# Optimization experiments

Measured on AMD Instinct MI355X. Metric: run time of the kernel, lower is better.

## Reference

```python
import math
import jax, jax.numpy as jnp
import numpy as np

B, C, K, P, STRIDE, ITERS = 32, 32, 3, 4, 2, 3
PSIZE = P * P
EPS = 1e-6
LAMBDA = 1e-3
LN_2PI = math.log(2.0 * math.pi)


def _extract_patches(x, K, stride):
    # Replicates torch F.unfold + transpose + view exactly, including the
    # layout reinterpretation: unfold's channel dim is ordered (c, kh, kw)
    # (c slowest) but the torch code views it as (K*K, c).
    b, h, w, c = x.shape
    pad = K // 2
    oh = (h + 2 * pad - K) // stride + 1
    ow = (w + 2 * pad - K) // stride + 1
    xp = jnp.pad(x, ((0, 0), (pad, pad), (pad, pad), (0, 0)))
    sl = []
    for kh in range(K):
        for kw in range(K):
            sl.append(xp[:, kh:kh + stride * (oh - 1) + 1:stride,
                            kw:kw + stride * (ow - 1) + 1:stride, :])
    p = jnp.stack(sl, axis=-1)                 # (b, oh, ow, c, K*K)  -> (c, kh, kw) order
    p = p.reshape(b, oh, ow, c * K * K)        # flat, c slowest (matches torch unfold memory)
    patches = p.reshape(b, oh, ow, K * K, c)   # reinterpret as (K*K, c), as the torch view does
    return patches, oh, ow


def _em_routing(v, a_in, beta_u, beta_a):
    # v: (b, Bin, C, psize), a_in: (b, Bin, 1)
    b, Bin, Cc, psize = v.shape
    r = jnp.full((b, Bin, Cc, 1), 1.0 / Cc, dtype=v.dtype)
    a4 = a_in[:, :, None, :]                   # (b, Bin, 1, 1)
    a_out = None
    mu = None
    for t in range(ITERS):
        # ---- M step ----
        rr = r * a4
        rr = rr / (jnp.sum(rr, axis=2, keepdims=True) + EPS)
        r_sum = jnp.sum(rr, axis=1, keepdims=True)            # (b,1,C,1)
        coeff = rr / (r_sum + EPS)
        mu = jnp.sum(coeff * v, axis=1, keepdims=True)        # (b,1,C,psize)
        sigma_sq = jnp.sum(coeff * (v - mu) ** 2, axis=1, keepdims=True) + EPS
        sigma_sq = jnp.maximum(sigma_sq, 1e-4)
        r_sum_flat = r_sum.reshape(b, Cc, 1)
        sig_flat = jnp.maximum(sigma_sq.reshape(b, Cc, psize), 1e-4)
        cost_h = (beta_u.reshape(1, Cc, 1) + jnp.log(jnp.sqrt(sig_flat))) * r_sum_flat
        a_out = jax.nn.sigmoid(LAMBDA * (beta_a.reshape(1, Cc) - jnp.sum(cost_h, axis=2)))
        a_out = jnp.clip(a_out, 1e-4, 1.0 - 1e-4)
        mu = jnp.nan_to_num(mu, nan=0.0, posinf=1e4, neginf=-1e4)
        sigma_sq = jnp.nan_to_num(sigma_sq, nan=1e-4, posinf=1e4, neginf=1e-4)
        a_out = jnp.nan_to_num(a_out, nan=0.5, posinf=1.0 - 1e-4, neginf=1e-4)
        # ---- E step ----
        if t < ITERS - 1:
            ss = jnp.maximum(sigma_sq, 1e-4)
            ao = jnp.clip(a_out, 1e-4, 1.0 - 1e-4)
            ln_p = -(v - mu) ** 2 / (2.0 * ss) - jnp.log(jnp.sqrt(ss)) - 0.5 * LN_2PI
            ln_ap = jnp.sum(ln_p, axis=3) + jnp.log(ao.reshape(b, 1, Cc) + EPS)
            ln_ap = jnp.nan_to_num(ln_ap, nan=0.0, posinf=50.0, neginf=-50.0)
            r = jax.nn.softmax(ln_ap, axis=2)[..., None]
            r = jnp.nan_to_num(r, nan=1.0 / Cc, posinf=1.0, neginf=0.0)
    p_out = jnp.nan_to_num(mu[:, 0], nan=0.0, posinf=1e4, neginf=-1e4)  # (b, C, psize)
    a_out = jnp.nan_to_num(a_out, nan=0.5, posinf=1.0 - 1e-4, neginf=1e-4)
    return p_out, a_out


def setup_inputs() -> dict:
    key = jax.random.key(0)
    k1, k2 = jax.random.split(key)
    x = jax.random.normal(k1, (2, 16, 16, B * (PSIZE + 1)), dtype=jnp.float32)
    weights = jax.random.normal(k2, (1, K * K * B, C, PSIZE, PSIZE), dtype=jnp.float32) * 0.02
    beta_u = jnp.zeros((C,), dtype=jnp.float32)
    beta_a = jnp.zeros((C,), dtype=jnp.float32)
    return {"x": x, "weights": weights, "beta_u": beta_u, "beta_a": beta_a}


def reference(x, weights, beta_u, beta_a):
    b, h, w, c = x.shape
    patches, oh, ow = _extract_patches(x, K, STRIDE)          # (b,oh,ow,K*K,c)
    p_in = patches[..., :B * PSIZE].reshape(b * oh * ow, K * K * B, PSIZE)
    a_in = patches[..., B * PSIZE:].reshape(b * oh * ow, K * K * B, 1)
    w0 = weights[0]                                           # (K*K*B, C, psize, psize)
    v = jnp.einsum('bip,icpq->bicq', p_in, w0)                # (b*, K*K*B, C, psize)
    p_out, a_out = _em_routing(v, a_in, beta_u, beta_a)
    p_out = p_out.reshape(b, oh, ow, C * PSIZE)
    a_out = a_out.reshape(b, oh, ow, C)
    out = jnp.concatenate([p_out, a_out], axis=3)
    return p_out, a_out, out
```

## Files before the change

kernel.cpp:

```cpp
#include <hip/hip_runtime.h>
#include <hip/hip_bf16.h>
#include <math.h>

#define EPSV 1e-6f
#define LAMBDAV 1e-3f
#define LN_2PI 1.8378770664093453f

__device__ __forceinline__ float bflo(unsigned int u) {
    union { unsigned int i; float f; } x; x.i = u << 16; return x.f;
}
__device__ __forceinline__ float bfhi(unsigned int u) {
    union { unsigned int i; float f; } x; x.i = u & 0xffff0000u; return x.f;
}
__device__ __forceinline__ unsigned short f2bf(float f) {
    __hip_bfloat16 h = __float2bfloat16(f);
    return *(unsigned short*)&h;
}

typedef __attribute__((ext_vector_type(8))) short s8v;
typedef __attribute__((ext_vector_type(4))) float f4v;

__global__ __launch_bounds__(256)
void conv_v_kernel(const float* __restrict__ x, const float* __restrict__ w,
                   __hip_bfloat16* __restrict__ vout)
{
    __shared__ unsigned short wb[512 * 40];
    __shared__ unsigned short pb[128 * 40];

    const int i2  = blockIdx.x;
    const int tid = threadIdx.x;

    for (int u = tid; u < 512 * 8; u += 256) {
        int r = u >> 3, j = u & 7;
        *(unsigned int*)&wb[r * 40 + 16 + j * 2] = 0;
    }
    for (int u = tid; u < 128 * 8; u += 256) {
        int r = u >> 3, j = u & 7;
        *(unsigned int*)&pb[r * 40 + 16 + j * 2] = 0;
    }
    #pragma unroll 4
    for (int u = 0; u < 32; ++u) {
        int idx = u * 256 + tid;
        int c = idx >> 8, p = (idx >> 4) & 15, q = idx & 15;
        wb[(c * 16 + q) * 40 + p] = f2bf(w[(size_t)i2 * 8192 + idx]);
    }
    #pragma unroll
    for (int u = 0; u < 8; ++u) {
        int idx = u * 256 + tid;
        int nn = idx >> 4, p = idx & 15;
        int e  = i2 * 16 + p;
        int k2 = e >> 9, c2 = e & 511;
        int f  = k2 * 544 + c2;
        int ci = f / 9, kk = f - ci * 9;
        int bi = nn >> 6, oi = (nn >> 3) & 7, oj = nn & 7;
        int row = 2 * oi + kk / 3 - 1;
        int col = 2 * oj + (kk - (kk / 3) * 3) - 1;
        float val = 0.f;
        if ((unsigned)row < 16u && (unsigned)col < 16u)
            val = x[((bi * 16 + row) * 16 + col) * 544 + ci];
        pb[nn * 40 + p] = f2bf(val);
    }
    __syncthreads();

    const int lane = tid & 63;
    const int wv   = tid >> 6;
    const int l16  = lane & 15;
    const int quad = lane >> 4;
    const int cq0  = wv * 128;

    s8v afrag[8], bfrag[8];
    #pragma unroll
    for (int mt = 0; mt < 8; ++mt)
        afrag[mt] = *(const s8v*)&wb[(cq0 + mt * 16 + l16) * 40 + quad * 8];
    #pragma unroll
    for (int nt = 0; nt < 8; ++nt)
        bfrag[nt] = *(const s8v*)&pb[(nt * 16 + l16) * 40 + quad * 8];

    #pragma unroll
    for (int nt = 0; nt < 8; ++nt) {
        const int nl = nt * 16 + l16;
        #pragma unroll
        for (int mt = 0; mt < 8; ++mt) {
            f4v acc = {0.f, 0.f, 0.f, 0.f};
            acc = __builtin_amdgcn_mfma_f32_16x16x32_bf16(afrag[mt], bfrag[nt], acc, 0, 0, 0);
            int cq = cq0 + mt * 16 + quad * 4;
            unsigned int lo = f2bf(acc[0]) | ((unsigned int)f2bf(acc[1]) << 16);
            unsigned int hi = f2bf(acc[2]) | ((unsigned int)f2bf(acc[3]) << 16);
            uint2 pk; pk.x = lo; pk.y = hi;
            *(uint2*)((unsigned short*)vout + ((size_t)nl * 288 + i2) * 512 + cq) = pk;
        }
    }
}

__global__ __launch_bounds__(1024, 4)
void em_routing_kernel(const float* __restrict__ x,
                       const unsigned short* __restrict__ v,
                       const float* __restrict__ beta_u,
                       const float* __restrict__ beta_a,
                       float* __restrict__ out)
{
    __shared__ float fct_s[288];
    __shared__ float red_s[16 * 64 * 17];
    __shared__ float mu_s[32 * 17];
    __shared__ float i2ss_s[32 * 17];
    __shared__ float hlog_s[32 * 17];
    __shared__ float rsum_s[32];
    __shared__ float aout_s[32];
    __shared__ float kc_s[32];

    const int n   = blockIdx.x;
    const int tid = threadIdx.x;
    const int bi = n >> 6, oi = (n >> 3) & 7, oj = n & 7;

    if (tid < 288) {
        int k2 = tid >> 5;
        int c2 = 512 + (tid & 31);
        int f  = k2 * 544 + c2;
        int ci = f / 9;
        int kk = f - ci * 9;
        int row = 2 * oi + kk / 3 - 1;
        int col = 2 * oj + (kk - (kk / 3) * 3) - 1;
        float a = 0.f;
        if ((unsigned)row < 16u && (unsigned)col < 16u)
            a = x[((bi * 16 + row) * 16 + col) * 544 + ci];
        fct_s[tid] = a / (a + EPSV);
    }
    __syncthreads();

    const unsigned short* vb = v + (size_t)n * 288 * 512;
    const int wv   = tid >> 6;
    const int lane = tid & 63;
    const int c    = lane & 31;
    const int qh   = lane >> 5;
    const int qb   = qh * 8;
    const unsigned short* base = vb + c * 16 + qb;

    for (int t = 0; t < 3; ++t) {
        float mu8[8], is8[8], kcv = 0.f;
        if (t > 0) {
            #pragma unroll
            for (int j = 0; j < 8; ++j) {
                mu8[j] = mu_s[c * 17 + qb + j];
                is8[j] = i2ss_s[c * 17 + qb + j];
            }
            kcv = kc_s[c];
        }

        float s0 = 0.f, s1[8], s2[8];
        #pragma unroll
        for (int j = 0; j < 8; ++j) { s1[j] = 0.f; s2[j] = 0.f; }

        uint4 ua = *(const uint4*)(base + (size_t)(0 * 16 + wv) * 512);
        uint4 ub = *(const uint4*)(base + (size_t)(1 * 16 + wv) * 512);

        for (int kp = 0; kp < 9; ++kp) {
            const int ia = (2 * kp) * 16 + wv;
            const int ib = (2 * kp + 1) * 16 + wv;
            uint4 una, unb;
            if (kp < 8) {
                una = *(const uint4*)(base + (size_t)((2 * kp + 2) * 16 + wv) * 512);
                unb = *(const uint4*)(base + (size_t)((2 * kp + 3) * 16 + wv) * 512);
            }
            float va[8], vvb[8];
            va[0] = bflo(ua.x); va[1] = bfhi(ua.x);
            va[2] = bflo(ua.y); va[3] = bfhi(ua.y);
            va[4] = bflo(ua.z); va[5] = bfhi(ua.z);
            va[6] = bflo(ua.w); va[7] = bfhi(ua.w);
            vvb[0] = bflo(ub.x); vvb[1] = bfhi(ub.x);
            vvb[2] = bflo(ub.y); vvb[3] = bfhi(ub.y);
            vvb[4] = bflo(ub.z); vvb[5] = bfhi(ub.z);
            vvb[6] = bflo(ub.w); vvb[7] = bfhi(ub.w);

            float rra, rrb;
            if (t == 0) {
                rra = fct_s[ia] * 0.03125f;
                rrb = fct_s[ib] * 0.03125f;
            } else {
                float pa = 0.f, pb2 = 0.f;
                #pragma unroll
                for (int j = 0; j < 8; ++j) {
                    float da = va[j] - mu8[j];
                    float db = vvb[j] - mu8[j];
                    pa  += da * da * is8[j];
                    pb2 += db * db * is8[j];
                }
                pa  += __shfl_xor(pa, 32, 64);
                pb2 += __shfl_xor(pb2, 32, 64);
                float acca = kcv - pa;
                float accb = kcv - pb2;
                float mxa = acca, mxb = accb;
                mxa = fmaxf(mxa, __shfl_xor(mxa, 1, 32));  mxb = fmaxf(mxb, __shfl_xor(mxb, 1, 32));
                mxa = fmaxf(mxa, __shfl_xor(mxa, 2, 32));  mxb = fmaxf(mxb, __shfl_xor(mxb, 2, 32));
                mxa = fmaxf(mxa, __shfl_xor(mxa, 4, 32));  mxb = fmaxf(mxb, __shfl_xor(mxb, 4, 32));
                mxa = fmaxf(mxa, __shfl_xor(mxa, 8, 32));  mxb = fmaxf(mxb, __shfl_xor(mxb, 8, 32));
                mxa = fmaxf(mxa, __shfl_xor(mxa, 16, 32)); mxb = fmaxf(mxb, __shfl_xor(mxb, 16, 32));
                float ea = __expf(acca - mxa);
                float eb = __expf(accb - mxb);
                float sa = ea, sb = eb;
                sa += __shfl_xor(sa, 1, 32);  sb += __shfl_xor(sb, 1, 32);
                sa += __shfl_xor(sa, 2, 32);  sb += __shfl_xor(sb, 2, 32);
                sa += __shfl_xor(sa, 4, 32);  sb += __shfl_xor(sb, 4, 32);
                sa += __shfl_xor(sa, 8, 32);  sb += __shfl_xor(sb, 8, 32);
                sa += __shfl_xor(sa, 16, 32); sb += __shfl_xor(sb, 16, 32);
                rra = (ea / sa) * fct_s[ia];
                rrb = (eb / sb) * fct_s[ib];
            }

            s0 += rra + rrb;
            #pragma unroll
            for (int j = 0; j < 8; ++j) {
                s1[j] += rra * va[j] + rrb * vvb[j];
                s2[j] += rra * va[j] * va[j] + rrb * vvb[j] * vvb[j];
            }
            ua = una; ub = unb;
        }

        {
            float* dst = &red_s[(wv * 64 + lane) * 17];
            dst[0] = s0;
            #pragma unroll
            for (int j = 0; j < 8; ++j) { dst[1 + j] = s1[j]; dst[9 + j] = s2[j]; }
        }
        __syncthreads();

        if (tid < 512) {
            int c2 = tid >> 4, q2 = tid & 15;
            int qh2 = q2 >> 3, j2 = q2 & 7;
            float S0 = 0.f, S1 = 0.f, S2 = 0.f;
            #pragma unroll
            for (int wvi = 0; wvi < 16; ++wvi) {
                S0 += red_s[(wvi * 64 + c2) * 17];
                const float* sp = &red_s[(wvi * 64 + qh2 * 32 + c2) * 17];
                S1 += sp[1 + j2];
                S2 += sp[9 + j2];
            }
            if (q2 == 0) rsum_s[c2] = S0;
            float invr = 1.0f / (S0 + EPSV);
            float w0  = S0 * invr;
            float m   = S1 * invr;
            float s2p = S2 * invr;
            float sig = s2p - m * m * (2.0f - w0);
            sig = fmaxf(sig + EPSV, 1e-4f);
            float hl = 0.5f * logf(sig);
            mu_s[c2 * 17 + q2]   = m;
            hlog_s[c2 * 17 + q2] = hl;
            i2ss_s[c2 * 17 + q2] = 1.0f / (2.0f * sig);
        }
        __syncthreads();

        if (tid < 32) {
            float cs = 0.f, shl = 0.f;
            float bu = beta_u[tid];
            #pragma unroll
            for (int q = 0; q < 16; ++q) { float hl = hlog_s[tid * 17 + q]; shl += hl; cs += bu + hl; }
            cs *= rsum_s[tid];
            float arg = LAMBDAV * (beta_a[tid] - cs);
            float ao  = 1.0f / (1.0f + expf(-arg));
            ao = fminf(fmaxf(ao, 1e-4f), 1.0f - 1e-4f);
            aout_s[tid] = ao;
            kc_s[tid]   = logf(ao + EPSV) - shl - 8.0f * LN_2PI;
        }
        __syncthreads();
    }

    if (tid < 512) {
        int c2 = tid >> 4, q2 = tid & 15;
        float mu = mu_s[c2 * 17 + q2];
        if (isnan(mu)) mu = 0.f;
        mu = fminf(fmaxf(mu, -10000.f), 10000.f);
        out[(size_t)n * 512 + tid] = mu;
        out[69632 + (size_t)n * 544 + tid] = mu;
        if (tid < 32) {
            float ao = aout_s[tid];
            if (isnan(ao)) ao = 0.5f;
            out[65536 + n * 32 + tid] = ao;
            out[69632 + n * 544 + 512 + tid] = ao;
        }
    }
}

extern "C" void kernel_launch(void* const* d_in, const int* in_sizes, int n_in,
                              void* d_out, int out_size, void* d_ws, size_t ws_size,
                              hipStream_t stream) {
    const float* x  = (const float*)d_in[0];
    const float* w  = (const float*)d_in[1];
    const float* bu = (const float*)d_in[2];
    const float* ba = (const float*)d_in[3];
    float* out = (float*)d_out;
    __hip_bfloat16* v = (__hip_bfloat16*)d_ws;

    conv_v_kernel<<<dim3(288), dim3(256), 0, stream>>>(x, w, v);
    em_routing_kernel<<<dim3(128), dim3(1024), 0, stream>>>(
        x, (const unsigned short*)v, bu, ba, out);
}
```

Measured before the change: 130.8 us.

## Remap EM routing lanes to full capsule vectors and use DPP reductions

Each lane now handles all 16 pose elements of one output capsule for a single input row, with the two wave halves processing alternate rows. Before, lanes split the pose elements in half and each covered two rows. This removes the cross-half shuffle inside the softmax, replaces shuffle-based 32-lane max/sum reductions with DPP moves plus a ds_swizzle, and folds the per-capsule activation computation into the 512-thread reduction through a 16-lane DPP sum, which drops one __syncthreads per iteration. The cost is higher register pressure from 16-element accumulators and an extra cross-half shuffle reduction of 33 values before writing to shared memory.

Measured after the change: 131.2 us. About the same (+0.3%).

```diff
diff --git a/kernel.cpp b/kernel.cpp
--- a/kernel.cpp
+++ b/kernel.cpp
@@ -19,6 +19,35 @@
 
 typedef __attribute__((ext_vector_type(8))) short s8v;
 typedef __attribute__((ext_vector_type(4))) float f4v;
+
+template<int CTRL>
+__device__ __forceinline__ float dpp_mv(float x) {
+    return __int_as_float(__builtin_amdgcn_update_dpp(
+        0, __float_as_int(x), CTRL, 0xF, 0xF, true));
+}
+__device__ __forceinline__ float red_max32(float x) {
+    x = fmaxf(x, dpp_mv<0xB1>(x));
+    x = fmaxf(x, dpp_mv<0x4E>(x));
+    x = fmaxf(x, dpp_mv<0x124>(x));
+    x = fmaxf(x, dpp_mv<0x128>(x));
+    x = fmaxf(x, __int_as_float(__builtin_amdgcn_ds_swizzle(__float_as_int(x), 0x401F)));
+    return x;
+}
+__device__ __forceinline__ float red_sum32(float x) {
+    x += dpp_mv<0xB1>(x);
+    x += dpp_mv<0x4E>(x);
+    x += dpp_mv<0x124>(x);
+    x += dpp_mv<0x128>(x);
+    x += __int_as_float(__builtin_amdgcn_ds_swizzle(__float_as_int(x), 0x401F));
+    return x;
+}
+__device__ __forceinline__ float red_sum16(float x) {
+    x += dpp_mv<0xB1>(x);
+    x += dpp_mv<0x4E>(x);
+    x += dpp_mv<0x124>(x);
+    x += dpp_mv<0x128>(x);
+    return x;
+}
 
 __global__ __launch_bounds__(256)
 void conv_v_kernel(const float* __restrict__ x, const float* __restrict__ w,
@@ -100,11 +129,9 @@
                        float* __restrict__ out)
 {
     __shared__ float fct_s[288];
-    __shared__ float red_s[16 * 64 * 17];
+    __shared__ float red_s[16 * 32 * 34];
     __shared__ float mu_s[32 * 17];
     __shared__ float i2ss_s[32 * 17];
-    __shared__ float hlog_s[32 * 17];
-    __shared__ float rsum_s[32];
     __shared__ float aout_s[32];
     __shared__ float kc_s[32];
 
@@ -131,110 +158,96 @@
     const int wv   = tid >> 6;
     const int lane = tid & 63;
     const int c    = lane & 31;
-    const int qh   = lane >> 5;
-    const int qb   = qh * 8;
-    const unsigned short* base = vb + c * 16 + qb;
+    const int half = lane >> 5;
+    const unsigned short* base = vb + c * 16;
 
     for (int t = 0; t < 3; ++t) {
-        float mu8[8], is8[8], kcv = 0.f;
+        float mu16[16], is16[16], kcv = 0.f;
         if (t > 0) {
             #pragma unroll
-            for (int j = 0; j < 8; ++j) {
-                mu8[j] = mu_s[c * 17 + qb + j];
-                is8[j] = i2ss_s[c * 17 + qb + j];
+            for (int j = 0; j < 16; ++j) {
+                mu16[j] = mu_s[c * 17 + j];
+                is16[j] = i2ss_s[c * 17 + j];
             }
             kcv = kc_s[c];
         }
 
-        float s0 = 0.f, s1[8], s2[8];
+        float s0 = 0.f, s1[16], s2[16];
         #pragma unroll
-        for (int j = 0; j < 8; ++j) { s1[j] = 0.f; s2[j] = 0.f; }
-
-        uint4 ua = *(const uint4*)(base + (size_t)(0 * 16 + wv) * 512);
-        uint4 ub = *(const uint4*)(base + (size_t)(1 * 16 + wv) * 512);
+        for (int j = 0; j < 16; ++j) { s1[j] = 0.f; s2[j] = 0.f; }
+
+        uint4 ua = *(const uint4*)(base + (size_t)(half * 16 + wv) * 512);
+        uint4 ub = *(const uint4*)(base + (size_t)(half * 16 + wv) * 512 + 8);
 
         for (int kp = 0; kp < 9; ++kp) {
-            const int ia = (2 * kp) * 16 + wv;
-            const int ib = (2 * kp + 1) * 16 + wv;
+            const int r = (2 * kp + half) * 16 + wv;
             uint4 una, unb;
             if (kp < 8) {
-                una = *(const uint4*)(base + (size_t)((2 * kp + 2) * 16 + wv) * 512);
-                unb = *(const uint4*)(base + (size_t)((2 * kp + 3) * 16 + wv) * 512);
-            }
-            float va[8], vvb[8];
-            va[0] = bflo(ua.x); va[1] = bfhi(ua.x);
-            va[2] = bflo(ua.y); va[3] = bfhi(ua.y);
-            va[4] = bflo(ua.z); va[5] = bfhi(ua.z);
-            va[6] = bflo(ua.w); va[7] = bfhi(ua.w);
-            vvb[0] = bflo(ub.x); vvb[1] = bfhi(ub.x);
-            vvb[2] = bflo(ub.y); vvb[3] = bfhi(ub.y);
-            vvb[4] = bflo(ub.z); vvb[5] = bfhi(ub.z);
-            vvb[6] = bflo(ub.w); vvb[7] = bfhi(ub.w);
-
-            float rra, rrb;
+                const int rn = (2 * kp + 2 + half) * 16 + wv;
+                una = *(const uint4*)(base + (size_t)rn * 512);
+                unb = *(const uint4*)(base + (size_t)rn * 512 + 8);
+            }
+            float va[16];
+            va[0]  = bflo(ua.x); va[1]  = bfhi(ua.x);
+            va[2]  = bflo(ua.y); va[3]  = bfhi(ua.y);
+            va[4]  = bflo(ua.z); va[5]  = bfhi(ua.z);
+            va[6]  = bflo(ua.w); va[7]  = bfhi(ua.w);
+            va[8]  = bflo(ub.x); va[9]  = bfhi(ub.x);
+            va[10] = bflo(ub.y); va[11] = bfhi(ub.y);
+            va[12] = bflo(ub.z); va[13] = bfhi(ub.z);
+            va[14] = bflo(ub.w); va[15] = bfhi(ub.w);
+
+            const float fct = fct_s[r];
+            float rra;
             if (t == 0) {
-                rra = fct_s[ia] * 0.03125f;
-                rrb = fct_s[ib] * 0.03125f;
+                rra = fct * 0.03125f;
             } else {
-                float pa = 0.f, pb2 = 0.f;
+                float pa = 0.f;
                 #pragma unroll
-                for (int j = 0; j < 8; ++j) {
-                    float da = va[j] - mu8[j];
-                    float db = vvb[j] - mu8[j];
-                    pa  += da * da * is8[j];
-                    pb2 += db * db * is8[j];
+                for (int j = 0; j < 16; ++j) {
+                    float d = va[j] - mu16[j];
+                    pa += d * d * is16[j];
                 }
-                pa  += __shfl_xor(pa, 32, 64);
-                pb2 += __shfl_xor(pb2, 32, 64);
-                float acca = kcv - pa;
-                float accb = kcv - pb2;
-                float mxa = acca, mxb = accb;
-                mxa = fmaxf(mxa, __shfl_xor(mxa, 1, 32));  mxb = fmaxf(mxb, __shfl_xor(mxb, 1, 32));
-                mxa = fmaxf(mxa, __shfl_xor(mxa, 2, 32));  mxb = fmaxf(mxb, __shfl_xor(mxb, 2, 32));
-                mxa = fmaxf(mxa, __shfl_xor(mxa, 4, 32));  mxb = fmaxf(mxb, __shfl_xor(mxb, 4, 32));
-                mxa = fmaxf(mxa, __shfl_xor(mxa, 8, 32));  mxb = fmaxf(mxb, __shfl_xor(mxb, 8, 32));
-                mxa = fmaxf(mxa, __shfl_xor(mxa, 16, 32)); mxb = fmaxf(mxb, __shfl_xor(mxb, 16, 32));
-                float ea = __expf(acca - mxa);
-                float eb = __expf(accb - mxb);
-                float sa = ea, sb = eb;
-                sa += __shfl_xor(sa, 1, 32);  sb += __shfl_xor(sb, 1, 32);
-                sa += __shfl_xor(sa, 2, 32);  sb += __shfl_xor(sb, 2, 32);
-                sa += __shfl_xor(sa, 4, 32);  sb += __shfl_xor(sb, 4, 32);
-                sa += __shfl_xor(sa, 8, 32);  sb += __shfl_xor(sb, 8, 32);
-                sa += __shfl_xor(sa, 16, 32); sb += __shfl_xor(sb, 16, 32);
-                rra = (ea / sa) * fct_s[ia];
-                rrb = (eb / sb) * fct_s[ib];
-            }
-
-            s0 += rra + rrb;
+                float acc = kcv - pa;
+                float mx = red_max32(acc);
+                float e  = __expf(acc - mx);
+                float sm = red_sum32(e);
+                rra = (e / sm) * fct;
+            }
+
+            s0 += rra;
             #pragma unroll
-            for (int j = 0; j < 8; ++j) {
-                s1[j] += rra * va[j] + rrb * vvb[j];
-                s2[j] += rra * va[j] * va[j] + rrb * vvb[j] * vvb[j];
+            for (int j = 0; j < 16; ++j) {
+                s1[j] += rra * va[j];
+                s2[j] += rra * va[j] * va[j];
             }
             ua = una; ub = unb;
         }
 
-        {
-            float* dst = &red_s[(wv * 64 + lane) * 17];
+        s0 += __shfl_xor(s0, 32, 64);
+        #pragma unroll
+        for (int j = 0; j < 16; ++j) {
+            s1[j] += __shfl_xor(s1[j], 32, 64);
+            s2[j] += __shfl_xor(s2[j], 32, 64);
+        }
+        if (half == 0) {
+            float* dst = &red_s[(wv * 32 + c) * 34];
             dst[0] = s0;
             #pragma unroll
-            for (int j = 0; j < 8; ++j) { dst[1 + j] = s1[j]; dst[9 + j] = s2[j]; }
+            for (int j = 0; j < 16; ++j) { dst[1 + j] = s1[j]; dst[17 + j] = s2[j]; }
         }
         __syncthreads();
 
         if (tid < 512) {
-            int c2 = tid >> 4, q2 = tid & 15;
-            int qh2 = q2 >> 3, j2 = q2 & 7;
+            const int c2 = tid >> 4, q2 = tid & 15;
             float S0 = 0.f, S1 = 0.f, S2 = 0.f;
             #pragma unroll
             for (int wvi = 0; wvi < 16; ++wvi) {
-                S0 += red_s[(wvi * 64 + c2) * 17];
-                const float* sp = &red_s[(wvi * 64 + qh2 * 32 + c2) * 17];
-                S1 += sp[1 + j2];
-                S2 += sp[9 + j2];
-            }
-            if (q2 == 0) rsum_s[c2] = S0;
+                const float* sp = &red_s[(wvi * 32 + c2) * 34];
+                S0 += sp[0];
+                S1 += sp[1 + q2];
+                S2 += sp[17 + q2];
+            }
             float invr = 1.0f / (S0 + EPSV);
             float w0  = S0 * invr;
             float m   = S1 * invr;
@@ -243,22 +256,17 @@
             sig = fmaxf(sig + EPSV, 1e-4f);
             float hl = 0.5f * logf(sig);
             mu_s[c2 * 17 + q2]   = m;
-            hlog_s[c2 * 17 + q2] = hl;
             i2ss_s[c2 * 17 + q2] = 1.0f / (2.0f * sig);
-        }
-        __syncthreads();
-
-        if (tid < 32) {
-            float cs = 0.f, shl = 0.f;
-            float bu = beta_u[tid];
-            #pragma unroll
-            for (int q = 0; q < 16; ++q) { float hl = hlog_s[tid * 17 + q]; shl += hl; cs += bu + hl; }
-            cs *= rsum_s[tid];
-            float arg = LAMBDAV * (beta_a[tid] - cs);
-            float ao  = 1.0f / (1.0f + expf(-arg));
-            ao = fminf(fmaxf(ao, 1e-4f), 1.0f - 1e-4f);
-            aout_s[tid] = ao;
-            kc_s[tid]   = logf(ao + EPSV) - shl - 8.0f * LN_2PI;
+            float shl = red_sum16(hl);
+            if (q2 == 0) {
+                float bu  = beta_u[c2];
+                float cs  = (16.0f * bu + shl) * S0;
+                float arg = LAMBDAV * (beta_a[c2] - cs);
+                float ao  = 1.0f / (1.0f + expf(-arg));
+                ao = fminf(fmaxf(ao, 1e-4f), 1.0f - 1e-4f);
+                aout_s[c2] = ao;
+                kc_s[c2]   = logf(ao + EPSV) - shl - 8.0f * LN_2PI;
+            }
         }
         __syncthreads();
     }
```
